# Performance work log

Hardware: AMD Instinct MI355X
Metric: run time of the kernel (lower is better)

Reference implementation:

```python
import math
import jax, jax.numpy as jnp
import numpy as np

SR = 48000
FRAME = 240
TWO_PI = 2.0 * math.pi


def _forward(B_inh, f0_offset, A0, tau1, tau2, a1, beat_hz, beat_depth, noise,
             f0, width_factor, duration_s):
    n_samples = int(duration_s * SR)
    T = int(math.ceil(n_samples / FRAME)) * FRAME
    Bb, K = A0.shape

    # --- inharmonic partial frequencies ---
    f0_adj = f0 * 2.0 ** (f0_offset / 1200.0)                      # (B,)
    k = jnp.arange(1, K + 1, dtype=f0.dtype)                       # (K,)
    f_k = f0_adj[:, None] * k[None, :] * jnp.sqrt(1.0 + B_inh[:, None] * k[None, :] ** 2)
    f_kb = f_k + beat_hz                                           # (B,K)

    t = jnp.arange(T, dtype=f0.dtype) / SR                         # (T,)

    # --- two-stage exponential amplitude envelope, (B,K,T) ---
    env = A0[:, :, None] * (a1[:, :, None] * jnp.exp(-t / tau1[:, :, None])
                            + (1.0 - a1[:, :, None]) * jnp.exp(-t / tau2[:, :, None]))

    # fixed random phases (original uses a seeded generator)
    pk = jax.random.split(jax.random.key(42), 3)
    phi_m = jax.random.uniform(pk[0], (Bb, K)) * TWO_PI
    phi_b = jax.random.uniform(pk[1], (Bb, K)) * TWO_PI

    osc = (jnp.cos(TWO_PI * f_k[:, :, None] * t + phi_m[:, :, None])
           + beat_depth[:, :, None] * jnp.cos(TWO_PI * f_kb[:, :, None] * t + phi_b[:, :, None]))

    harmonic = jnp.sum(env * osc, axis=1)                          # (B,T)
    peak = jnp.clip(jnp.max(jnp.abs(harmonic), axis=1, keepdims=True), 1e-6, None)
    harmonic = harmonic / peak * 0.9

    # --- coloured noise: one-pole IIR via parallel associative scan ---
    attack_tau = noise[:, 0:1]                                     # (B,1)
    floor_rms = noise[:, 1:2]                                      # (B,1)
    centroid = noise[:, 2]                                         # (B,)
    nyq = SR / 2.0
    f_lo = 27.5
    log_range = math.log2(nyq / f_lo)
    cutoff = jnp.clip(f_lo * 2.0 ** (centroid * log_range) / nyq, 0.01, 0.99)
    pole = jnp.exp(-TWO_PI * cutoff)                               # (B,)
    alpha = 1.0 - pole

    white = jax.random.normal(pk[2], (Bb, T), dtype=f0.dtype)
    # x_i = pole * x_{i-1} + alpha * w_i  -> affine composition scan over time
    a = jnp.broadcast_to(pole[None, :], (T, Bb))                   # (T,B)
    b = alpha[None, :] * white.T                                   # (T,B)

    def comb(x, y):
        return (x[0] * y[0], x[1] * y[0] + y[1])

    _, filt = jax.lax.associative_scan(comb, (a, b), axis=0)
    noise_env = jnp.exp(-t[None, :] / jnp.clip(attack_tau, 0.002, None)) * floor_rms
    noise_sig = filt.T * noise_env                                 # (B,T)

    mono = (harmonic + noise_sig)[:, :n_samples]
    w = jnp.clip(width_factor, 0.0, 2.0)[:, None]
    side = mono * w * 0.3
    left = jnp.clip(mono + side, -1.0, 1.0)
    right = jnp.clip(mono - side, -1.0, 1.0)
    return jnp.stack([left, right], axis=1)                        # (B,2,n_samples)


def setup_inputs() -> dict:
    key = jax.random.key(0)
    B, K = 4, 64
    ks = jax.random.split(key, 12)
    f0 = jax.random.uniform(ks[0], (B,), minval=65.0, maxval=880.0)
    B_inh = jax.random.uniform(ks[1], (B,)) * 1e-4          # piano inharmonicity
    f0_offset = jax.random.normal(ks[2], (B,)) * 5.0        # cents
    A0 = jax.random.uniform(ks[3], (B, K))
    tau1 = jax.random.uniform(ks[4], (B, K)) * 0.4 + 0.05   # fast decay (s)
    tau2 = jax.random.uniform(ks[5], (B, K)) * 2.0 + 0.5    # slow decay (s)
    a1 = jax.random.uniform(ks[6], (B, K))
    beat_hz = jax.random.uniform(ks[7], (B, K)) * 2.0
    beat_depth = jax.random.uniform(ks[8], (B, K)) * 0.3
    noise = jnp.stack([
        jax.random.uniform(ks[9], (B,)) * 0.1 + 0.01,   # attack_tau
        jax.random.uniform(ks[10], (B,)) * 0.01,        # floor_rms
        jax.random.uniform(ks[11], (B,)),               # centroid_norm
        jnp.zeros((B,)),                                # slope_db_oct (unused)
    ], axis=1)
    width_factor = jnp.ones((B,))
    return dict(B_inh=B_inh, f0_offset=f0_offset, A0=A0, tau1=tau1, tau2=tau2,
                a1=a1, beat_hz=beat_hz, beat_depth=beat_depth, noise=noise,
                f0=f0, width_factor=width_factor, duration_s=3)


def reference(B_inh, f0_offset, A0, tau1, tau2, a1, beat_hz, beat_depth, noise,
              f0, width_factor, duration_s):
    return _forward(B_inh, f0_offset, A0, tau1, tau2, a1, beat_hz, beat_depth,
                    noise, f0, width_factor, duration_s)
```

## Files before the change

### kernel.cpp

```cpp
#include <hip/hip_runtime.h>
#include <stdint.h>
#include <math.h>

#pragma clang fp contract(off)

#define B_BATCH 4
#define K_HARM  64
#define T_TOT   144000
#define N_SAMP  144000
#define WF      128

#define OFF_PK    0
#define PK_STRIDE 16
#define OFF_POLE  4096
#define OFF_ALPHA 4100
#define OFF_AT    4104
#define OFF_FR    4108
#define OFF_WC    4112
#define OFF_PEAK  4116
#define OFF_HARM  4128

static constexpr float  TWO_PI_F = 6.28318530717958647692f;
static constexpr double INV2PI_D = 0.15915494309189535;
static constexpr float  C_HI = (float)INV2PI_D;
static constexpr float  C_LO = (float)(INV2PI_D - (double)((float)INV2PI_D));
static constexpr float  LOG2E_F = 1.44269504088896340736f;
static constexpr float  LN2_F   = 0.69314718055994530942f;

__device__ __forceinline__ uint32_t rotl32(uint32_t x, uint32_t n) {
    return (x << n) | (x >> (32u - n));
}

__device__ __forceinline__ void tf2x32(uint32_t k0, uint32_t k1, uint32_t x0, uint32_t x1,
                                       uint32_t& o0, uint32_t& o1) {
    const uint32_t ks2 = k0 ^ k1 ^ 0x1BD11BDAu;
    x0 += k0; x1 += k1;
#define TF_RND(r) { x0 += x1; x1 = rotl32(x1, (r)); x1 ^= x0; }
    TF_RND(13) TF_RND(15) TF_RND(26) TF_RND(6)
    x0 += k1;  x1 += ks2 + 1u;
    TF_RND(17) TF_RND(29) TF_RND(16) TF_RND(24)
    x0 += ks2; x1 += k0 + 2u;
    TF_RND(13) TF_RND(15) TF_RND(26) TF_RND(6)
    x0 += k0;  x1 += k1 + 3u;
    TF_RND(17) TF_RND(29) TF_RND(16) TF_RND(24)
    x0 += k1;  x1 += ks2 + 4u;
    TF_RND(13) TF_RND(15) TF_RND(26) TF_RND(6)
    x0 += ks2; x1 += k0 + 5u;
#undef TF_RND
    o0 = x0; o1 = x1;
}

__device__ __forceinline__ void get_keys(uint32_t pk[3][2]) {
    tf2x32(0u, 42u, 0u, 0u, pk[0][0], pk[0][1]);
    tf2x32(0u, 42u, 0u, 1u, pk[1][0], pk[1][1]);
    tf2x32(0u, 42u, 0u, 2u, pk[2][0], pk[2][1]);
}

__device__ __forceinline__ uint32_t bits_for(const uint32_t key[2], uint32_t idx) {
    uint32_t o0, o1;
    tf2x32(key[0], key[1], 0u, idx, o0, o1);
    return o0 ^ o1;
}

__device__ __forceinline__ float u01_from_bits(uint32_t bits) {
    return __fsub_rn(__uint_as_float((bits >> 9) | 0x3f800000u), 1.0f);
}

__device__ __forceinline__ float erfinv_fast(float x) {
    float v = fmaf(-x, x, 1.0f);
    float w = __fmul_rn(-LN2_F, __builtin_amdgcn_logf(v));
    float p;
    if (w < 5.0f) {
        w = __fsub_rn(w, 2.5f);
        p = 2.81022636e-08f;
        p = fmaf(p, w, 3.43273939e-07f);
        p = fmaf(p, w, -3.5233877e-06f);
        p = fmaf(p, w, -4.39150654e-06f);
        p = fmaf(p, w, 0.00021858087f);
        p = fmaf(p, w, -0.00125372503f);
        p = fmaf(p, w, -0.00417768164f);
        p = fmaf(p, w, 0.246640727f);
        p = fmaf(p, w, 1.50140941f);
    } else {
        w = __fsub_rn(sqrtf(w), 3.0f);
        p = -0.000200214257f;
        p = fmaf(p, w, 0.000100950558f);
        p = fmaf(p, w, 0.00134934322f);
        p = fmaf(p, w, -0.00367342844f);
        p = fmaf(p, w, 0.00573950773f);
        p = fmaf(p, w, -0.0076224613f);
        p = fmaf(p, w, 0.00943887047f);
        p = fmaf(p, w, 1.00167406f);
        p = fmaf(p, w, 2.83297682f);
    }
    return __fmul_rn(p, x);
}

__device__ __forceinline__ float normal_from_bits(uint32_t bits) {
    const float LO = __uint_as_float(0xBF7FFFFFu);
    float f = u01_from_bits(bits);
    float u = __fadd_rn(__fmul_rn(f, 2.0f), LO);
    u = fmaxf(u, LO);
    const float SQRT2_F = 1.41421356237309504880f;
    return __fmul_rn(SQRT2_F, erfinv_fast(u));
}

__device__ __forceinline__ float reduce_rev(float arg) {
    float p = __fmul_rn(arg, C_HI);
    float e = fmaf(arg, C_HI, -p);
    float n = rintf(p);
    float r = __fadd_rn(__fsub_rn(p, n), e);
    return fmaf(arg, C_LO, r);
}

__global__ void kprep(const float* __restrict__ B_inh, const float* __restrict__ f0_off,
                      const float* __restrict__ beat_hz, const float* __restrict__ noise,
                      const float* __restrict__ f0, const float* __restrict__ wfac,
                      const float* __restrict__ A0, const float* __restrict__ tau1,
                      const float* __restrict__ tau2, const float* __restrict__ a1,
                      const float* __restrict__ bd,
                      float* __restrict__ ws) {
    int j = threadIdx.x;
    uint32_t pk[3][2];
    get_keys(pk);

    float phim = __fmul_rn(u01_from_bits(bits_for(pk[0], (uint32_t)j)), TWO_PI_F);
    float phib = __fmul_rn(u01_from_bits(bits_for(pk[1], (uint32_t)j)), TWO_PI_F);

    int b = j >> 6;
    int k = (j & 63) + 1;
    float x   = __fdiv_rn(f0_off[b], 1200.0f);
    float s   = (float)exp2((double)x);
    float f0a = __fmul_rn(f0[b], s);
    float sq  = sqrtf(__fadd_rn(1.0f, __fmul_rn(B_inh[b], (float)(k * k))));
    float fk  = __fmul_rn(__fmul_rn(f0a, (float)k), sq);
    float fkb = __fadd_rn(fk, beat_hz[j]);

    float w_  = __fmul_rn(TWO_PI_F, fk);
    float wb_ = __fmul_rn(TWO_PI_F, fkb);
    float c1  = __fdiv_rn(-LOG2E_F, __fmul_rn(48000.0f, tau1[j]));
    float c2  = __fdiv_rn(-LOG2E_F, __fmul_rn(48000.0f, tau2[j]));

    float* P = ws + OFF_PK + j * PK_STRIDE;
    P[0] = w_;
    P[1] = wb_;
    P[2] = phim;
    P[3] = phib;
    P[4] = c1;
    P[5] = c2;
    float a1v = a1[j];
    P[6] = __fmul_rn(A0[j], a1v);
    P[7] = __fmul_rn(A0[j], __fsub_rn(1.0f, a1v));
    P[8] = bd[j];
    double dth  = (double)w_  / 48000.0;
    double dthb = (double)wb_ / 48000.0;
    P[9]  = (float)cos(dth);
    P[10] = (float)sin(dth);
    P[11] = (float)cos(dthb);
    P[12] = (float)sin(dthb);
    P[13] = (float)exp2((double)c1);
    P[14] = (float)exp2((double)c2);

    if (j < B_BATCH) {
        float at  = fmaxf(noise[j * 4 + 0], 0.002f);
        float fr  = noise[j * 4 + 1];
        float cen = noise[j * 4 + 2];
        float lr  = (float)log2(24000.0 / 27.5);
        float y   = __fmul_rn(cen, lr);
        float e   = (float)exp2((double)y);
        float v   = __fdiv_rn(__fmul_rn(27.5f, e), 24000.0f);
        float cut = fminf(fmaxf(v, 0.01f), 0.99f);
        float pole = expf(__fmul_rn(-TWO_PI_F, cut));
        ws[OFF_POLE + j]  = pole;
        ws[OFF_ALPHA + j] = __fsub_rn(1.0f, pole);
        ws[OFF_AT + j] = at;
        ws[OFF_FR + j] = fr;
        ws[OFF_WC + j] = fminf(fmaxf(wfac[j], 0.0f), 2.0f);
        ((unsigned int*)ws)[OFF_PEAK + j] = 0u;
    }
}

#define SPT_H 8
#define TBLK  512
#define RROW  528

__global__ void kharm(const float* __restrict__ prm,
                      float* __restrict__ harm,
                      unsigned int* __restrict__ peak) {
    __shared__ float red[4][RROW];
    __shared__ float mxs[4];
    const int tid  = threadIdx.x;
    const int lane = tid & 63;
    const int kq   = __builtin_amdgcn_readfirstlane(tid >> 6);
    const int b    = blockIdx.y;
    const int t0b  = blockIdx.x * TBLK;
    const int t0   = t0b + lane * SPT_H;

    const float fn0 = (float)t0;
    const float tt0 = __fdiv_rn(fn0, 48000.0f);

    float acc[SPT_H];
#pragma unroll
    for (int j = 0; j < SPT_H; ++j) acc[j] = 0.0f;

    const float* Pb = prm + OFF_PK + (((b << 6) + (kq << 4)) * PK_STRIDE);

#pragma unroll 2
    for (int kk = 0; kk < 16; ++kk) {
        const float* P = Pb + kk * PK_STRIDE;
        float w  = P[0], wb2 = P[1], pm = P[2], pb = P[3];
        float c1 = P[4], c2 = P[5], A1 = P[6], A2 = P[7], bdk = P[8];
        float cdm = P[9], sdm = P[10], cdb = P[11], sdb = P[12];
        float d1 = P[13], d2 = P[14];

        float am = __fadd_rn(__fmul_rn(w,   tt0), pm);
        float ab = __fadd_rn(__fmul_rn(wb2, tt0), pb);
        float rm = reduce_rev(am);
        float rb = reduce_rev(ab);
        float cm = __builtin_amdgcn_cosf(rm), sm = __builtin_amdgcn_sinf(rm);
        float cb = __builtin_amdgcn_cosf(rb), sb = __builtin_amdgcn_sinf(rb);

        float xm  = cm;
        float xpm = fmaf(sm, sdm, __fmul_rn(cm, cdm));
        float xb  = __fmul_rn(bdk, cb);
        float xpb = __fmul_rn(bdk, fmaf(sb, sdb, __fmul_rn(cb, cdb)));
        float km  = __fadd_rn(cdm, cdm);
        float kb2 = __fadd_rn(cdb, cdb);
        float e1  = __fmul_rn(A1, __builtin_amdgcn_exp2f(__fmul_rn(fn0, c1)));
        float e2  = __fmul_rn(A2, __builtin_amdgcn_exp2f(__fmul_rn(fn0, c2)));

#pragma unroll
        for (int j = 0; j < SPT_H; ++j) {
            float env = __fadd_rn(e1, e2);
            float osc = __fadd_rn(xm, xb);
            acc[j] = fmaf(env, osc, acc[j]);
            if (j < SPT_H - 1) {
                float xn  = fmaf(km,  xm, -xpm); xpm = xm; xm = xn;
                float xbn = fmaf(kb2, xb, -xpb); xpb = xb; xb = xbn;
                e1 = __fmul_rn(e1, d1);
                e2 = __fmul_rn(e2, d2);
            }
        }
    }

#pragma unroll
    for (int j = 0; j < SPT_H; ++j) {
        int c = lane * SPT_H + j;
        red[kq][c + (c >> 5)] = acc[j];
    }
    __syncthreads();

    int c0 = tid * 2;
    int c1i = c0 + 1;
    float s0 = 0.0f, s1 = 0.0f;
#pragma unroll
    for (int q = 0; q < 4; ++q) {
        s0 = __fadd_rn(s0, red[q][c0  + (c0  >> 5)]);
        s1 = __fadd_rn(s1, red[q][c1i + (c1i >> 5)]);
    }
    int tg = t0b + c0;
    float m = 0.0f;
    if (tg < T_TOT) {
        *(float2*)(harm + b * T_TOT + tg) = make_float2(s0, s1);
        m = fmaxf(fabsf(s0), fabsf(s1));
    }
#pragma unroll
    for (int off = 32; off > 0; off >>= 1)
        m = fmaxf(m, __shfl_xor(m, off));
    if (lane == 0) mxs[tid >> 6] = m;
    __syncthreads();
    if (tid == 0) {
        float mm = fmaxf(fmaxf(mxs[0], mxs[1]), fmaxf(mxs[2], mxs[3]));
        atomicMax(&peak[b], __float_as_uint(mm));
    }
}

#define SPT   4
#define CHUNK 1024
#define WIN   (CHUNK + WF - 1)

__global__ void kfinal(const float* __restrict__ ws, float* __restrict__ out) {
    __shared__ __align__(16) float s[WIN + 1];
    __shared__ __align__(16) float ptab[WF];
    const int b   = blockIdx.y;
    const int t0  = blockIdx.x * CHUNK;
    const int tid = threadIdx.x;

    const float alpha = ws[OFF_ALPHA + b];
    const float pole  = ws[OFF_POLE + b];
    const float at    = ws[OFF_AT + b];
    const float fr    = ws[OFF_FR + b];
    const float wcf   = ws[OFF_WC + b];
    const float peak  = fmaxf(__uint_as_float(((const unsigned int*)ws)[OFF_PEAK + b]), 1e-6f);
    const float cpk   = __fdiv_rn(0.9f, peak);

    uint32_t k2a, k2b;
    tf2x32(0u, 42u, 0u, 2u, k2a, k2b);

    for (int idx = tid; idx < WIN; idx += 256) {
        int j = t0 - (WF - 1) + idx;
        float v = 0.0f;
        if (j >= 0 && j < T_TOT) {
            uint32_t o0, o1;
            tf2x32(k2a, k2b, 0u, (uint32_t)(b * T_TOT + j), o0, o1);
            v = __fmul_rn(alpha, normal_from_bits(o0 ^ o1));
        }
        s[idx] = v;
    }
    if (tid < WF) ptab[tid] = exp2f((float)tid * log2f(pole));
    __syncthreads();

    const int t = t0 + tid * SPT;
    if (t >= N_SAMP) return;
    const float p128 = __fmul_rn(ptab[WF - 1], pole);
    const int base = tid * SPT + (WF - 1);

    float f0 = 0.f, f1 = 0.f, f2 = 0.f, f3 = 0.f;
#pragma unroll
    for (int m4 = 0; m4 < WF / 4; ++m4) {
        float4 p4 = *(const float4*)&ptab[m4 * 4];
        float4 s4 = *(const float4*)&s[base - m4 * 4 - 3];
        f0 = fmaf(p4.x, s4.w, f0);
        f1 = fmaf(p4.y, s4.z, f1);
        f2 = fmaf(p4.z, s4.y, f2);
        f3 = fmaf(p4.w, s4.x, f3);
    }
    float filt = __fadd_rn(__fadd_rn(f0, f2), __fadd_rn(f1, f3));

    const float4 h4 = *(const float4*)(ws + OFF_HARM + b * T_TOT + t);
    float* outL = out + (b * 2 + 0) * N_SAMP;
    float* outR = out + (b * 2 + 1) * N_SAMP;

    float tt  = __fdiv_rn((float)t, 48000.0f);
    float ne  = __fmul_rn(__expf(__fdiv_rn(-tt, at)), fr);
    const float ned = __expf(__fdiv_rn(-1.0f, __fmul_rn(48000.0f, at)));

    float4 L, R;
    const float hv[4] = {h4.x, h4.y, h4.z, h4.w};
    float lv[4], rv[4];
#pragma unroll
    for (int jj = 0; jj < SPT; ++jj) {
        if (jj > 0) {
            filt = fmaf(pole, filt, s[base + jj]);
            filt = fmaf(-p128, s[base + jj - WF], filt);
            ne   = __fmul_rn(ne, ned);
        }
        float hn   = __fmul_rn(hv[jj], cpk);
        float ns   = __fmul_rn(filt, ne);
        float mono = __fadd_rn(hn, ns);
        float side = __fmul_rn(__fmul_rn(mono, wcf), 0.3f);
        lv[jj] = fminf(fmaxf(__fadd_rn(mono, side), -1.0f), 1.0f);
        rv[jj] = fminf(fmaxf(__fsub_rn(mono, side), -1.0f), 1.0f);
    }
    L = make_float4(lv[0], lv[1], lv[2], lv[3]);
    R = make_float4(rv[0], rv[1], rv[2], rv[3]);
    *(float4*)&outL[t] = L;
    *(float4*)&outR[t] = R;
}

extern "C" void kernel_launch(void* const* d_in, const int* in_sizes, int n_in,
                              void* d_out, int out_size, void* d_ws, size_t ws_size,
                              hipStream_t stream) {
    (void)in_sizes; (void)n_in; (void)out_size; (void)ws_size;
    const float* B_inh   = (const float*)d_in[0];
    const float* f0_off  = (const float*)d_in[1];
    const float* A0      = (const float*)d_in[2];
    const float* tau1    = (const float*)d_in[3];
    const float* tau2    = (const float*)d_in[4];
    const float* a1      = (const float*)d_in[5];
    const float* beat_hz = (const float*)d_in[6];
    const float* beat_dp = (const float*)d_in[7];
    const float* noise   = (const float*)d_in[8];
    const float* f0      = (const float*)d_in[9];
    const float* wfac    = (const float*)d_in[10];
    float* out = (float*)d_out;
    float* ws  = (float*)d_ws;

    kprep<<<dim3(1), dim3(256), 0, stream>>>(B_inh, f0_off, beat_hz, noise, f0, wfac,
                                             A0, tau1, tau2, a1, beat_dp, ws);

    dim3 gh((T_TOT + TBLK - 1) / TBLK, B_BATCH);
    kharm<<<gh, dim3(256), 0, stream>>>(ws, ws + OFF_HARM,
                                        (unsigned int*)ws + OFF_PEAK);

    dim3 gf((N_SAMP + CHUNK - 1) / CHUNK, B_BATCH);
    kfinal<<<gf, dim3(256), 0, stream>>>(ws, out);
}
```

Before: 34.22 us.

## Double samples per thread in harmonic kernel and use fast intrinsics in prep

The harmonic synthesis kernel now gives each thread 16 consecutive samples instead of 8 and uses 512-thread blocks. The 64 partials are split across 8 wavefront groups of 8, which cuts per-partial setup cost (range reduction, sin/cos seeding) relative to recurrence work and doubles the cross-group reduction in shared memory. The prep kernel replaces double-precision cos/sin/exp2 with hardware float intrinsics on a fractional revolution. This removes slow FP64 transcendental calls but lowers the precision of the per-sample rotation and decay factors. Longer recurrences of 16 steps may accumulate more drift.

```diff
diff --git a/kernel.cpp b/kernel.cpp
--- a/kernel.cpp
+++ b/kernel.cpp
@@ -152,14 +152,14 @@
     P[6] = __fmul_rn(A0[j], a1v);
     P[7] = __fmul_rn(A0[j], __fsub_rn(1.0f, a1v));
     P[8] = bd[j];
-    double dth  = (double)w_  / 48000.0;
-    double dthb = (double)wb_ / 48000.0;
-    P[9]  = (float)cos(dth);
-    P[10] = (float)sin(dth);
-    P[11] = (float)cos(dthb);
-    P[12] = (float)sin(dthb);
-    P[13] = (float)exp2((double)c1);
-    P[14] = (float)exp2((double)c2);
+    float revm = __fdiv_rn(fk,  48000.0f); revm = __fsub_rn(revm, floorf(revm));
+    float revb = __fdiv_rn(fkb, 48000.0f); revb = __fsub_rn(revb, floorf(revb));
+    P[9]  = __builtin_amdgcn_cosf(revm);
+    P[10] = __builtin_amdgcn_sinf(revm);
+    P[11] = __builtin_amdgcn_cosf(revb);
+    P[12] = __builtin_amdgcn_sinf(revb);
+    P[13] = __builtin_amdgcn_exp2f(c1);
+    P[14] = __builtin_amdgcn_exp2f(c2);
 
     if (j < B_BATCH) {
         float at  = fmaxf(noise[j * 4 + 0], 0.002f);
@@ -180,15 +180,16 @@
     }
 }
 
-#define SPT_H 8
-#define TBLK  512
-#define RROW  528
+#define SPT_H 16
+#define TBLK  1024
+#define KQ_N  8
+#define RROW  1056
 
 __global__ void kharm(const float* __restrict__ prm,
                       float* __restrict__ harm,
                       unsigned int* __restrict__ peak) {
-    __shared__ float red[4][RROW];
-    __shared__ float mxs[4];
+    __shared__ float red[KQ_N][RROW];
+    __shared__ float mxs[KQ_N];
     const int tid  = threadIdx.x;
     const int lane = tid & 63;
     const int kq   = __builtin_amdgcn_readfirstlane(tid >> 6);
@@ -203,10 +204,10 @@
 #pragma unroll
     for (int j = 0; j < SPT_H; ++j) acc[j] = 0.0f;
 
-    const float* Pb = prm + OFF_PK + (((b << 6) + (kq << 4)) * PK_STRIDE);
+    const float* Pb = prm + OFF_PK + (((b << 6) + (kq << 3)) * PK_STRIDE);
 
 #pragma unroll 2
-    for (int kk = 0; kk < 16; ++kk) {
+    for (int kk = 0; kk < K_HARM / KQ_N; ++kk) {
         const float* P = Pb + kk * PK_STRIDE;
         float w  = P[0], wb2 = P[1], pm = P[2], pb = P[3];
         float c1 = P[4], c2 = P[5], A1 = P[6], A2 = P[7], bdk = P[8];
@@ -250,17 +251,17 @@
     }
     __syncthreads();
 
-    int c0 = tid * 2;
+    int c0  = tid * 2;
     int c1i = c0 + 1;
-    float s0 = 0.0f, s1 = 0.0f;
-#pragma unroll
-    for (int q = 0; q < 4; ++q) {
-        s0 = __fadd_rn(s0, red[q][c0  + (c0  >> 5)]);
-        s1 = __fadd_rn(s1, red[q][c1i + (c1i >> 5)]);
-    }
-    int tg = t0b + c0;
+    int tg  = t0b + c0;
     float m = 0.0f;
     if (tg < T_TOT) {
+        float s0 = 0.0f, s1 = 0.0f;
+#pragma unroll
+        for (int q = 0; q < KQ_N; ++q) {
+            s0 = __fadd_rn(s0, red[q][c0  + (c0  >> 5)]);
+            s1 = __fadd_rn(s1, red[q][c1i + (c1i >> 5)]);
+        }
         *(float2*)(harm + b * T_TOT + tg) = make_float2(s0, s1);
         m = fmaxf(fabsf(s0), fabsf(s1));
     }
@@ -270,7 +271,9 @@
     if (lane == 0) mxs[tid >> 6] = m;
     __syncthreads();
     if (tid == 0) {
-        float mm = fmaxf(fmaxf(mxs[0], mxs[1]), fmaxf(mxs[2], mxs[3]));
+        float mm = mxs[0];
+#pragma unroll
+        for (int q = 1; q < KQ_N; ++q) mm = fmaxf(mm, mxs[q]);
         atomicMax(&peak[b], __float_as_uint(mm));
     }
 }
@@ -335,7 +338,6 @@
     float ne  = __fmul_rn(__expf(__fdiv_rn(-tt, at)), fr);
     const float ned = __expf(__fdiv_rn(-1.0f, __fmul_rn(48000.0f, at)));
 
-    float4 L, R;
     const float hv[4] = {h4.x, h4.y, h4.z, h4.w};
     float lv[4], rv[4];
 #pragma unroll
@@ -352,10 +354,8 @@
         lv[jj] = fminf(fmaxf(__fadd_rn(mono, side), -1.0f), 1.0f);
         rv[jj] = fminf(fmaxf(__fsub_rn(mono, side), -1.0f), 1.0f);
     }
-    L = make_float4(lv[0], lv[1], lv[2], lv[3]);
-    R = make_float4(rv[0], rv[1], rv[2], rv[3]);
-    *(float4*)&outL[t] = L;
-    *(float4*)&outR[t] = R;
+    *(float4*)&outL[t] = make_float4(lv[0], lv[1], lv[2], lv[3]);
+    *(float4*)&outR[t] = make_float4(rv[0], rv[1], rv[2], rv[3]);
 }
 
 extern "C" void kernel_launch(void* const* d_in, const int* in_sizes, int n_in,
@@ -380,7 +380,7 @@
                                              A0, tau1, tau2, a1, beat_dp, ws);
 
     dim3 gh((T_TOT + TBLK - 1) / TBLK, B_BATCH);
-    kharm<<<gh, dim3(256), 0, stream>>>(ws, ws + OFF_HARM,
+    kharm<<<gh, dim3(512), 0, stream>>>(ws, ws + OFF_HARM,
                                         (unsigned int*)ws + OFF_PEAK);
 
     dim3 gf((N_SAMP + CHUNK - 1) / CHUNK, B_BATCH);
```

Measured after the change: 28.73 us. 16.1% less time.
